# Kernel optimization log

Hardware: AMD Instinct MI355X
Metric: run time of the kernel (lower is better)

Reference implementation:

```python
import jax, jax.numpy as jnp
import numpy as np

MAX_DIM = 1024
VOCAB = 257
DEPTH = 6
Q_DIM = MAX_DIM // 4  # 256
EXP_DIMS = [1, 2, 4, 8, 16, 32, 64, 128]  # expander sizes: current_q doubles up to Q_DIM
BATCH, SEQ = 8, 4096


def qlinear(q, W):
    """Quaternion Hamilton-product linear.
    q: [..., in, 4] (last dim = r,i,j,k components), W: [4, out, in] (stacked r,i,j,k weights).
    Returns [..., out, 4].
    """
    # P[..., o, w, a] = F.linear(component_a, W_w)  -> all 16 small GEMMs in one einsum
    P = jnp.einsum('...ia,woi->...owa', q, W)
    Pr, Pi, Pj, Pk = P[..., 0, :], P[..., 1, :], P[..., 2, :], P[..., 3, :]  # each [..., out, 4]
    out_r = Pr[..., 0] - Pi[..., 1] - Pj[..., 2] - Pk[..., 3]
    out_i = Pi[..., 0] + Pr[..., 1] + Pk[..., 2] - Pj[..., 3]
    out_j = Pj[..., 0] - Pk[..., 1] + Pr[..., 2] + Pi[..., 3]
    out_k = Pk[..., 0] + Pj[..., 1] - Pi[..., 2] + Pr[..., 3]
    return jnp.stack([out_r, out_i, out_j, out_k], axis=-1)


def qnormalize(q):
    norm = jnp.linalg.norm(q, axis=-1, keepdims=True)
    return q / (norm + 1e-8)


def setup_inputs() -> dict:
    key = jax.random.key(0)
    ks = jax.random.split(key, 4 + len(EXP_DIMS))
    inp = {}
    inp['x'] = jax.random.randint(ks[0], (BATCH, SEQ), 0, VOCAB)
    inp['emb'] = jax.random.normal(ks[1], (VOCAB, 4), dtype=jnp.float32)
    for idx, cq in enumerate(EXP_DIMS):
        scale = cq ** (-0.5)
        inp[f'w_exp{idx}'] = jax.random.uniform(ks[2 + idx], (4, cq, cq), jnp.float32, -scale, scale)
    scale = Q_DIM ** (-0.5)
    inp['w_layers'] = jax.random.uniform(ks[-2], (DEPTH, 4, Q_DIM, Q_DIM), jnp.float32, -scale, scale)
    inp['w_head'] = jax.random.normal(ks[-1], (VOCAB, MAX_DIM), dtype=jnp.float32) * MAX_DIM ** (-0.5)
    return inp


def reference(x, emb, w_exp0, w_exp1, w_exp2, w_exp3, w_exp4, w_exp5, w_exp6, w_exp7,
              w_layers, w_head):
    q = emb[x][:, :, None, :]  # [B, S, 1, 4]
    for w in (w_exp0, w_exp1, w_exp2, w_exp3, w_exp4, w_exp5, w_exp6, w_exp7):
        delta = jnp.tanh(qlinear(q, w))
        q = jnp.concatenate([q + delta, q - delta], axis=2)  # doubles quaternion dim
    for d in range(DEPTH):
        q = qnormalize(qlinear(q, w_layers[d]))
    stability_loss = jnp.mean(jnp.abs(q[..., 0]))
    h_flat = q.reshape(x.shape[0], x.shape[1], -1)  # [B, S, MAX_DIM]
    logits = jnp.einsum('bsd,vd->bsv', h_flat, w_head)
    return (logits, stability_loss)
```

## Files before the change

kernel.cpp:

```cpp
#include <hip/hip_runtime.h>


typedef _Float16 f16x8 __attribute__((ext_vector_type(8)));
typedef float    f32x4 __attribute__((ext_vector_type(4)));

#define GL2LDS16(gp, lp) __builtin_amdgcn_global_load_lds(                     \
    (const __attribute__((address_space(1))) void*)(gp),                       \
    (__attribute__((address_space(3))) void*)(lp), 16, 0, 0)

__device__ __forceinline__ unsigned short f2h(float f) {
  union { _Float16 h; unsigned short u; } c;
  c.h = (_Float16)f;
  return c.u;
}
__device__ __forceinline__ float h2f(unsigned short u) {
  union { unsigned short u; _Float16 h; } c;
  c.u = u;
  return (float)c.h;
}

__global__ __launch_bounds__(256) void expand_ham(
    const float* __restrict__ w, unsigned short* __restrict__ out,
    int cq, int kbits, int total) {
  int id = blockIdx.x * 256 + threadIdx.x;
  if (id >= total) return;
  const int K = 1 << kbits;
  const int n = id >> kbits;
  const int k = id & (K - 1);
  float val = 0.f;
  if (n < 4 * cq) {
    const int o = n >> 2, a = n & 3, i = k >> 2, b = k & 3;
    const int   comp[4][4] = {{0,1,2,3},{1,0,3,2},{2,3,0,1},{3,2,1,0}};
    const float sgn [4][4] = {{1.f,-1.f,-1.f,-1.f},{1.f,1.f,1.f,-1.f},
                              {1.f,-1.f,1.f,1.f},{1.f,1.f,-1.f,1.f}};
    val = sgn[a][b] * w[comp[a][b] * cq * cq + o * cq + i];
  }
  out[id] = f2h(val);
}

__global__ __launch_bounds__(256) void conv_head(
    const float* __restrict__ wh, unsigned short* __restrict__ out) {
  int id = blockIdx.x * 256 + threadIdx.x;
  int v = id >> 10, k = id & 1023;
  out[id] = f2h(v < 257 ? wh[v * 1024 + k] : 0.f);
}

template <int CQ>
__device__ __forceinline__ void exp_step(float (&q)[16][4],
                                         const float* __restrict__ w) {
  float d[CQ][4];
#pragma unroll
  for (int o = 0; o < CQ; o++) {
    float pr = 0.f, pi = 0.f, pj = 0.f, pk = 0.f;
#pragma unroll
    for (int i = 0; i < CQ; i++) {
      const float wr = w[0 * CQ * CQ + o * CQ + i];
      const float wi = w[1 * CQ * CQ + o * CQ + i];
      const float wj = w[2 * CQ * CQ + o * CQ + i];
      const float wk = w[3 * CQ * CQ + o * CQ + i];
      const float qr = q[i][0], qi = q[i][1], qj = q[i][2], qk = q[i][3];
      pr += wr * qr - wi * qi - wj * qj - wk * qk;
      pi += wi * qr + wr * qi + wk * qj - wj * qk;
      pj += wj * qr - wk * qi + wr * qj + wi * qk;
      pk += wk * qr + wj * qi - wi * qj + wr * qk;
    }
    d[o][0] = tanhf(pr); d[o][1] = tanhf(pi);
    d[o][2] = tanhf(pj); d[o][3] = tanhf(pk);
  }
#pragma unroll
  for (int o = 0; o < CQ; o++)
#pragma unroll
    for (int a = 0; a < 4; a++) {
      const float dd = d[o][a], qq = q[o][a];
      q[o][a]      = qq + dd;
      q[CQ + o][a] = qq - dd;
    }
}

__global__ __launch_bounds__(256) void embed_expand(
    const int* __restrict__ x, const float* __restrict__ emb,
    const float* __restrict__ w0, const float* __restrict__ w1,
    const float* __restrict__ w2, const float* __restrict__ w3,
    unsigned short* __restrict__ out) {
  const int t = blockIdx.x * 256 + threadIdx.x;
  float q[16][4];
  const int v = x[t];
  const float4 e = *(const float4*)(emb + v * 4);
  q[0][0] = e.x; q[0][1] = e.y; q[0][2] = e.z; q[0][3] = e.w;
  exp_step<1>(q, w0);
  exp_step<2>(q, w1);
  exp_step<4>(q, w2);
  exp_step<8>(q, w3);
  ushort4* o4 = (ushort4*)(out + (size_t)t * 64);
#pragma unroll
  for (int c = 0; c < 16; c++) {
    ushort4 u;
    u.x = f2h(q[c][0]); u.y = f2h(q[c][1]);
    u.z = f2h(q[c][2]); u.w = f2h(q[c][3]);
    o4[c] = u;
  }
}

template <int EPI>
__global__ __launch_bounds__(256) void gemm_epi(
    const unsigned short* __restrict__ W,
    const unsigned short* __restrict__ Act,
    unsigned short* __restrict__ OutB, float* __restrict__ OutF,
    int K, int Nreal, int ldout) {
  __shared__ unsigned short WtL[128 * 32];
  __shared__ unsigned short WtH[128 * 32];
  __shared__ unsigned short AtL[128 * 32];
  __shared__ unsigned short AtH[128 * 32];

  const int tid  = threadIdx.x;
  const int wave = tid >> 6;
  const int lane = tid & 63;
  const int l15  = lane & 15;
  const int quad = lane >> 4;

  const int Gx = gridDim.x;
  const int L  = blockIdx.y * Gx + blockIdx.x;
  const int j  = L & 7;
  const int s  = L >> 3;
  const int nblock = (s % Gx) * 128;
  const int mblock = (32 * j + s / Gx) * 128;
  const int wn = (wave & 1) * 64;
  const int wm = (wave >> 1) * 64;

  f32x4 acc[4][4];
  const f32x4 zero = {0.f, 0.f, 0.f, 0.f};
#pragma unroll
  for (int a = 0; a < 4; a++)
#pragma unroll
    for (int b = 0; b < 4; b++) acc[a][b] = zero;

  const int row0 = tid >> 2;
  const int sub  = tid & 3;
  const unsigned short* gW0 = W   + (size_t)(nblock + row0)      * K + sub * 8;
  const unsigned short* gW1 = W   + (size_t)(nblock + row0 + 64) * K + sub * 8;
  const unsigned short* gA0 = Act + (size_t)(mblock + row0)      * K + sub * 8;
  const unsigned short* gA1 = Act + (size_t)(mblock + row0 + 64) * K + sub * 8;
  unsigned short* lWL0 = &WtL[wave * 512];
  unsigned short* lWL1 = &WtL[2048 + wave * 512];
  unsigned short* lWH0 = &WtH[wave * 512];
  unsigned short* lWH1 = &WtH[2048 + wave * 512];
  unsigned short* lAL0 = &AtL[wave * 512];
  unsigned short* lAL1 = &AtL[2048 + wave * 512];
  unsigned short* lAH0 = &AtH[wave * 512];
  unsigned short* lAH1 = &AtH[2048 + wave * 512];

  for (int kb = 0; kb < K; kb += 64) {
    GL2LDS16(gW0 + kb,      lWL0);
    GL2LDS16(gW1 + kb,      lWL1);
    GL2LDS16(gW0 + kb + 32, lWH0);
    GL2LDS16(gW1 + kb + 32, lWH1);
    GL2LDS16(gA0 + kb,      lAL0);
    GL2LDS16(gA1 + kb,      lAL1);
    GL2LDS16(gA0 + kb + 32, lAH0);
    GL2LDS16(gA1 + kb + 32, lAH1);
    __syncthreads();

    {
      f16x8 afr[4], bfr[4];
#pragma unroll
      for (int tn = 0; tn < 4; tn++)
        afr[tn] = *(const f16x8*)&WtL[(wn + tn * 16 + l15) * 32 + quad * 8];
#pragma unroll
      for (int tm = 0; tm < 4; tm++)
        bfr[tm] = *(const f16x8*)&AtL[(wm + tm * 16 + l15) * 32 + quad * 8];
#pragma unroll
      for (int tn = 0; tn < 4; tn++)
#pragma unroll
        for (int tm = 0; tm < 4; tm++)
          acc[tn][tm] = __builtin_amdgcn_mfma_f32_16x16x32_f16(
              afr[tn], bfr[tm], acc[tn][tm], 0, 0, 0);
    }
    {
      f16x8 afr[4], bfr[4];
#pragma unroll
      for (int tn = 0; tn < 4; tn++)
        afr[tn] = *(const f16x8*)&WtH[(wn + tn * 16 + l15) * 32 + quad * 8];
#pragma unroll
      for (int tm = 0; tm < 4; tm++)
        bfr[tm] = *(const f16x8*)&AtH[(wm + tm * 16 + l15) * 32 + quad * 8];
#pragma unroll
      for (int tn = 0; tn < 4; tn++)
#pragma unroll
        for (int tm = 0; tm < 4; tm++)
          acc[tn][tm] = __builtin_amdgcn_mfma_f32_16x16x32_f16(
              afr[tn], bfr[tm], acc[tn][tm], 0, 0, 0);
    }
    __syncthreads();
  }

#pragma unroll
  for (int tn = 0; tn < 4; tn++) {
    const int n = nblock + wn + tn * 16 + quad * 4;
    if (n < Nreal) {
#pragma unroll
      for (int tm = 0; tm < 4; tm++) {
        const int token = mblock + wm + tm * 16 + l15;
        const f32x4 v = acc[tn][tm];
        const unsigned short* ip = Act + (size_t)token * K + n;
        const float i0 = h2f(ip[0]), i1 = h2f(ip[1]);
        const float i2 = h2f(ip[2]), i3 = h2f(ip[3]);
        const float d0 = tanhf(v[0]), d1 = tanhf(v[1]);
        const float d2 = tanhf(v[2]), d3 = tanhf(v[3]);
        ushort4 up, um;
        up.x = f2h(i0 + d0); up.y = f2h(i1 + d1);
        up.z = f2h(i2 + d2); up.w = f2h(i3 + d3);
        um.x = f2h(i0 - d0); um.y = f2h(i1 - d1);
        um.z = f2h(i2 - d2); um.w = f2h(i3 - d3);
        *(ushort4*)&OutB[(size_t)token * ldout + n] = up;
        *(ushort4*)&OutB[(size_t)token * ldout + Nreal + n] = um;
      }
    }
  }
}

template <int EPI>
__global__ __launch_bounds__(512, 4) void gemm8p(
    const unsigned short* __restrict__ W,
    const unsigned short* __restrict__ Act,
    unsigned short* __restrict__ OutB, float* __restrict__ OutF,
    int K, int NW, int ldout) {
  __shared__ unsigned short S[3 * 12288];
  __shared__ float lsum[8];

  const int tid  = threadIdx.x;
  const int wave = tid >> 6;
  const int lane = tid & 63;
  const int l15  = lane & 15;
  const int quad = lane >> 4;
  const int wr   = wave >> 2;
  const int wc   = wave & 3;

  const int Gx = gridDim.x;
  const int L  = blockIdx.y * Gx + blockIdx.x;
  const int j  = L & 7;
  const int s  = L >> 3;
  const int mblock = (j * (gridDim.y >> 3) + s / Gx) * 256;
  const int nblock = (s % Gx) * 128;
  const int NT = K >> 5;

  f32x4 acc[4][4];
  const f32x4 zero = {0.f, 0.f, 0.f, 0.f};
#pragma unroll
  for (int a = 0; a < 4; a++)
#pragma unroll
    for (int b = 0; b < 4; b++) acc[a][b] = zero;

  const int rw = tid >> 2;
  const int sl = (tid & 3) ^ ((tid >> 3) & 3);
  const int wrow = nblock + rw;
  const int cwr  = wrow < NW ? wrow : NW - 1;
  const unsigned short* sW  = W   + (size_t)cwr * K + sl * 8;
  const unsigned short* sB0 = Act + (size_t)(mblock + rw)       * K + sl * 8;
  const unsigned short* sB1 = Act + (size_t)(mblock + 128 + rw) * K + sl * 8;

  const int swz = (quad * 8) ^ ((l15 & 6) << 2);

#pragma unroll
  for (int t = 0; t < 2; ++t) {
    unsigned short* d = S + t * 12288 + tid * 8;
    GL2LDS16(sW  + t * 32, d);
    GL2LDS16(sB0 + t * 32, d + 4096);
    GL2LDS16(sB1 + t * 32, d + 8192);
  }
  asm volatile("s_waitcnt vmcnt(3)" ::: "memory");
  __builtin_amdgcn_s_barrier();
  __builtin_amdgcn_sched_barrier(0);

  int bC = 0;
  int bS = 2;
  for (int kt = 0; kt < NT; ++kt) {
    const unsigned short* SA = S + bC * 12288;
    const unsigned short* SB = SA + 4096;

    f16x8 af[4], bf[4];
#pragma unroll
    for (int t4 = 0; t4 < 4; t4++)
      af[t4] = *(const f16x8*)(SA + (wr * 64 + t4 * 16 + l15) * 32 + swz);
#pragma unroll
    for (int t4 = 0; t4 < 4; t4++)
      bf[t4] = *(const f16x8*)(SB + (wc * 64 + t4 * 16 + l15) * 32 + swz);

    if (kt + 2 < NT) {
      const int kb = (kt + 2) * 32;
      unsigned short* d = S + bS * 12288 + tid * 8;
      GL2LDS16(sW  + kb, d);
      GL2LDS16(sB0 + kb, d + 4096);
      GL2LDS16(sB1 + kb, d + 8192);
    }

    __builtin_amdgcn_s_barrier();
    asm volatile("s_waitcnt lgkmcnt(0)" ::: "memory");
    __builtin_amdgcn_sched_barrier(0);
    __builtin_amdgcn_s_setprio(1);
#pragma unroll
    for (int tn = 0; tn < 4; tn++)
#pragma unroll
      for (int tm = 0; tm < 4; tm++)
        acc[tn][tm] = __builtin_amdgcn_mfma_f32_16x16x32_f16(
            af[tn], bf[tm], acc[tn][tm], 0, 0, 0);
    __builtin_amdgcn_s_setprio(0);

    if (kt < NT - 1) {
      if (kt + 2 < NT) asm volatile("s_waitcnt vmcnt(3)" ::: "memory");
      else             asm volatile("s_waitcnt vmcnt(0)" ::: "memory");
      __builtin_amdgcn_s_barrier();
      __builtin_amdgcn_sched_barrier(0);
    }
    bC = bC == 2 ? 0 : bC + 1;
    bS = bS == 2 ? 0 : bS + 1;
  }

  if constexpr (EPI == 0) {
#pragma unroll
    for (int tn = 0; tn < 4; tn++) {
      const int n = nblock + wr * 64 + tn * 16 + quad * 4;
#pragma unroll
      for (int tm = 0; tm < 4; tm++) {
        const int token = mblock + wc * 64 + tm * 16 + l15;
        const f32x4 v = acc[tn][tm];
        const unsigned short* ip = Act + (size_t)token * K + n;
        const float i0 = h2f(ip[0]), i1 = h2f(ip[1]);
        const float i2 = h2f(ip[2]), i3 = h2f(ip[3]);
        const float d0 = tanhf(v[0]), d1 = tanhf(v[1]);
        const float d2 = tanhf(v[2]), d3 = tanhf(v[3]);
        ushort4 up, um;
        up.x = f2h(i0 + d0); up.y = f2h(i1 + d1);
        up.z = f2h(i2 + d2); up.w = f2h(i3 + d3);
        um.x = f2h(i0 - d0); um.y = f2h(i1 - d1);
        um.z = f2h(i2 - d2); um.w = f2h(i3 - d3);
        *(ushort4*)&OutB[(size_t)token * ldout + n] = up;
        *(ushort4*)&OutB[(size_t)token * ldout + NW + n] = um;
      }
    }
  } else if constexpr (EPI == 1 || EPI == 2) {
    float loss = 0.f;
#pragma unroll
    for (int tn = 0; tn < 4; tn++) {
      const int n = nblock + wr * 64 + tn * 16 + quad * 4;
#pragma unroll
      for (int tm = 0; tm < 4; tm++) {
        const int token = mblock + wc * 64 + tm * 16 + l15;
        const f32x4 v = acc[tn][tm];
        const float nrm =
            sqrtf(v[0] * v[0] + v[1] * v[1] + v[2] * v[2] + v[3] * v[3]);
        const float inv = 1.f / (nrm + 1e-8f);
        ushort4 u;
        u.x = f2h(v[0] * inv); u.y = f2h(v[1] * inv);
        u.z = f2h(v[2] * inv); u.w = f2h(v[3] * inv);
        *(ushort4*)&OutB[(size_t)token * 1024 + n] = u;
        if constexpr (EPI == 2) loss += fabsf(v[0] * inv);
      }
    }
    if constexpr (EPI == 2) {
#pragma unroll
      for (int off = 32; off > 0; off >>= 1) loss += __shfl_down(loss, off);
      if (lane == 0) lsum[wave] = loss;
      __syncthreads();
      if (tid == 0) {
        float t = 0.f;
#pragma unroll
        for (int w8 = 0; w8 < 8; w8++) t += lsum[w8];
        atomicAdd(OutF, t * (1.f / 8388608.f));
      }
    }
  } else {
#pragma unroll
    for (int tn = 0; tn < 4; tn++) {
      const int n = nblock + wr * 64 + tn * 16 + quad * 4;
      if (n < 257) {
#pragma unroll
        for (int tm = 0; tm < 4; tm++) {
          const int token = mblock + wc * 64 + tm * 16 + l15;
          const f32x4 v = acc[tn][tm];
#pragma unroll
          for (int r = 0; r < 4; r++)
            if (n + r < 257) OutF[(size_t)token * 257 + n + r] = v[r];
        }
      }
    }
  }
}

extern "C" void kernel_launch(void* const* d_in, const int* in_sizes, int n_in,
                              void* d_out, int out_size, void* d_ws,
                              size_t ws_size, hipStream_t stream) {
  const int*   x    = (const int*)d_in[0];
  const float* emb  = (const float*)d_in[1];
  const float* we0  = (const float*)d_in[2];
  const float* we1  = (const float*)d_in[3];
  const float* we2  = (const float*)d_in[4];
  const float* we3  = (const float*)d_in[5];
  const float* we4  = (const float*)d_in[6];
  const float* we5  = (const float*)d_in[7];
  const float* we6  = (const float*)d_in[8];
  const float* we7  = (const float*)d_in[9];
  const float* wlay = (const float*)d_in[10];
  const float* wh   = (const float*)d_in[11];
  float* out = (float*)d_out;

  char* p = (char*)d_ws;
  auto alloc = [&](size_t bytes) {
    void* r = (void*)p;
    p += (bytes + 255) & ~(size_t)255;
    return r;
  };
  unsigned short* act0 = (unsigned short*)alloc(32768ull * 1024 * 2);
  unsigned short* act1 = (unsigned short*)alloc(32768ull * 1024 * 2);
  unsigned short* E4 = (unsigned short*)alloc(128 * 64 * 2);
  unsigned short* E5 = (unsigned short*)alloc(128 * 128 * 2);
  unsigned short* E6 = (unsigned short*)alloc(256 * 256 * 2);
  unsigned short* E7 = (unsigned short*)alloc(512 * 512 * 2);
  unsigned short* EL = (unsigned short*)alloc(6ull * 1024 * 1024 * 2);
  unsigned short* WH = (unsigned short*)alloc(384 * 1024 * 2);

  hipMemsetAsync(out + 8421376, 0, 4, stream);

  expand_ham<<<dim3(8192 / 256), 256, 0, stream>>>(we4, E4, 16, 6, 128 * 64);
  expand_ham<<<dim3(16384 / 256), 256, 0, stream>>>(we5, E5, 32, 7, 128 * 128);
  expand_ham<<<dim3(65536 / 256), 256, 0, stream>>>(we6, E6, 64, 8, 256 * 256);
  expand_ham<<<dim3(262144 / 256), 256, 0, stream>>>(we7, E7, 128, 9,
                                                     512 * 512);
  for (int d = 0; d < 6; d++)
    expand_ham<<<dim3(1048576 / 256), 256, 0, stream>>>(
        wlay + (size_t)d * 262144, EL + (size_t)d * 1048576, 256, 10, 1048576);
  conv_head<<<dim3(384 * 1024 / 256), 256, 0, stream>>>(wh, WH);

  embed_expand<<<dim3(128), 256, 0, stream>>>(x, emb, we0, we1, we2, we3, act0);

  gemm_epi<0><<<dim3(1, 256), 256, 0, stream>>>(E4, act0, act1, nullptr, 64,
                                                64, 128);
  gemm_epi<0><<<dim3(1, 256), 256, 0, stream>>>(E5, act1, act0, nullptr, 128,
                                                128, 256);
  gemm8p<0><<<dim3(2, 128), 512, 0, stream>>>(E6, act0, act1, nullptr, 256,
                                              256, 512);
  gemm8p<0><<<dim3(4, 128), 512, 0, stream>>>(E7, act1, act0, nullptr, 512,
                                              512, 1024);

  unsigned short* a = act0;
  unsigned short* b = act1;
  for (int d = 0; d < 5; d++) {
    gemm8p<1><<<dim3(8, 128), 512, 0, stream>>>(EL + (size_t)d * 1048576, a, b,
                                                nullptr, 1024, 1024, 1024);
    unsigned short* t = a; a = b; b = t;
  }
  gemm8p<2><<<dim3(8, 128), 512, 0, stream>>>(EL + 5ull * 1048576, a, b,
                                              out + 8421376, 1024, 1024, 1024);
  { unsigned short* t = a; a = b; b = t; }

  gemm8p<3><<<dim3(3, 128), 512, 0, stream>>>(WH, a, nullptr, out, 1024, 384,
                                              0);
}
```

Before: 832.7 us.

## Shrink gemm8p tile to 128x128 with 4 waves and double-buffered LDS

Restructures the main GEMM kernel from 512-thread blocks on a 128x256 tile with triple-buffered LDS to 256-thread blocks on a 128x128 tile with double buffering. The grid doubles in the M dimension and each thread loads two W rows and two activation rows. The barrier now comes before the next prefetch so the buffer being refilled is safe. The aim is more resident blocks per CU and less LDS per block, at the cost of less reuse per tile and one fewer stage of prefetch slack. It also merges the six layer-weight expansion launches into a single kernel.

```diff
diff --git a/kernel.cpp b/kernel.cpp
--- a/kernel.cpp
+++ b/kernel.cpp
@@ -35,6 +35,21 @@
                               {1.f,-1.f,1.f,1.f},{1.f,1.f,-1.f,1.f}};
     val = sgn[a][b] * w[comp[a][b] * cq * cq + o * cq + i];
   }
+  out[id] = f2h(val);
+}
+
+__global__ __launch_bounds__(256) void expand_ham6(
+    const float* __restrict__ w, unsigned short* __restrict__ out) {
+  const int id = blockIdx.x * 256 + threadIdx.x;
+  const int d = id >> 20;
+  const int r = id & 1048575;
+  const int n = r >> 10, k = r & 1023;
+  const int o = n >> 2, a = n & 3, i = k >> 2, b = k & 3;
+  const int   comp[4][4] = {{0,1,2,3},{1,0,3,2},{2,3,0,1},{3,2,1,0}};
+  const float sgn [4][4] = {{1.f,-1.f,-1.f,-1.f},{1.f,1.f,1.f,-1.f},
+                            {1.f,-1.f,1.f,1.f},{1.f,1.f,-1.f,1.f}};
+  const float val =
+      sgn[a][b] * w[d * 262144 + comp[a][b] * 65536 + o * 256 + i];
   out[id] = f2h(val);
 }
 
@@ -219,27 +234,27 @@
 }
 
 template <int EPI>
-__global__ __launch_bounds__(512, 4) void gemm8p(
+__global__ __launch_bounds__(256, 4) void gemm8p(
     const unsigned short* __restrict__ W,
     const unsigned short* __restrict__ Act,
     unsigned short* __restrict__ OutB, float* __restrict__ OutF,
     int K, int NW, int ldout) {
-  __shared__ unsigned short S[3 * 12288];
-  __shared__ float lsum[8];
+  __shared__ unsigned short S[2 * 8192];
+  __shared__ float lsum[4];
 
   const int tid  = threadIdx.x;
   const int wave = tid >> 6;
   const int lane = tid & 63;
   const int l15  = lane & 15;
   const int quad = lane >> 4;
-  const int wr   = wave >> 2;
-  const int wc   = wave & 3;
+  const int wr   = wave >> 1;
+  const int wc   = wave & 1;
 
   const int Gx = gridDim.x;
   const int L  = blockIdx.y * Gx + blockIdx.x;
   const int j  = L & 7;
   const int s  = L >> 3;
-  const int mblock = (j * (gridDim.y >> 3) + s / Gx) * 256;
+  const int mblock = (j * (gridDim.y >> 3) + s / Gx) * 128;
   const int nblock = (s % Gx) * 128;
   const int NT = K >> 5;
 
@@ -252,29 +267,40 @@
 
   const int rw = tid >> 2;
   const int sl = (tid & 3) ^ ((tid >> 3) & 3);
-  const int wrow = nblock + rw;
-  const int cwr  = wrow < NW ? wrow : NW - 1;
-  const unsigned short* sW  = W   + (size_t)cwr * K + sl * 8;
-  const unsigned short* sB0 = Act + (size_t)(mblock + rw)       * K + sl * 8;
-  const unsigned short* sB1 = Act + (size_t)(mblock + 128 + rw) * K + sl * 8;
+  const int wrow0 = nblock + rw;
+  const int wrow1 = nblock + 64 + rw;
+  const int cw0 = wrow0 < NW ? wrow0 : NW - 1;
+  const int cw1 = wrow1 < NW ? wrow1 : NW - 1;
+  const unsigned short* sW0 = W   + (size_t)cw0 * K + sl * 8;
+  const unsigned short* sW1 = W   + (size_t)cw1 * K + sl * 8;
+  const unsigned short* sB0 = Act + (size_t)(mblock + rw)      * K + sl * 8;
+  const unsigned short* sB1 = Act + (size_t)(mblock + 64 + rw) * K + sl * 8;
 
   const int swz = (quad * 8) ^ ((l15 & 6) << 2);
 
-#pragma unroll
-  for (int t = 0; t < 2; ++t) {
-    unsigned short* d = S + t * 12288 + tid * 8;
-    GL2LDS16(sW  + t * 32, d);
-    GL2LDS16(sB0 + t * 32, d + 4096);
-    GL2LDS16(sB1 + t * 32, d + 8192);
-  }
-  asm volatile("s_waitcnt vmcnt(3)" ::: "memory");
+  {
+    unsigned short* d0 = S + tid * 8;
+    GL2LDS16(sW0, d0);
+    GL2LDS16(sW1, d0 + 2048);
+    GL2LDS16(sB0, d0 + 4096);
+    GL2LDS16(sB1, d0 + 6144);
+    if (NT > 1) {
+      unsigned short* d1 = S + 8192 + tid * 8;
+      GL2LDS16(sW0 + 32, d1);
+      GL2LDS16(sW1 + 32, d1 + 2048);
+      GL2LDS16(sB0 + 32, d1 + 4096);
+      GL2LDS16(sB1 + 32, d1 + 6144);
+      asm volatile("s_waitcnt vmcnt(4)" ::: "memory");
+    } else {
+      asm volatile("s_waitcnt vmcnt(0)" ::: "memory");
+    }
+  }
   __builtin_amdgcn_s_barrier();
   __builtin_amdgcn_sched_barrier(0);
 
-  int bC = 0;
-  int bS = 2;
+#pragma unroll 2
   for (int kt = 0; kt < NT; ++kt) {
-    const unsigned short* SA = S + bC * 12288;
+    const unsigned short* SA = S + (kt & 1) * 8192;
     const unsigned short* SB = SA + 4096;
 
     f16x8 af[4], bf[4];
@@ -285,17 +311,18 @@
     for (int t4 = 0; t4 < 4; t4++)
       bf[t4] = *(const f16x8*)(SB + (wc * 64 + t4 * 16 + l15) * 32 + swz);
 
+    asm volatile("s_waitcnt lgkmcnt(0)" ::: "memory");
+    __builtin_amdgcn_s_barrier();
+    __builtin_amdgcn_sched_barrier(0);
     if (kt + 2 < NT) {
       const int kb = (kt + 2) * 32;
-      unsigned short* d = S + bS * 12288 + tid * 8;
-      GL2LDS16(sW  + kb, d);
+      unsigned short* d = S + (kt & 1) * 8192 + tid * 8;
+      GL2LDS16(sW0 + kb, d);
+      GL2LDS16(sW1 + kb, d + 2048);
       GL2LDS16(sB0 + kb, d + 4096);
-      GL2LDS16(sB1 + kb, d + 8192);
-    }
-
-    __builtin_amdgcn_s_barrier();
-    asm volatile("s_waitcnt lgkmcnt(0)" ::: "memory");
-    __builtin_amdgcn_sched_barrier(0);
+      GL2LDS16(sB1 + kb, d + 6144);
+    }
+
     __builtin_amdgcn_s_setprio(1);
 #pragma unroll
     for (int tn = 0; tn < 4; tn++)
@@ -306,13 +333,11 @@
     __builtin_amdgcn_s_setprio(0);
 
     if (kt < NT - 1) {
-      if (kt + 2 < NT) asm volatile("s_waitcnt vmcnt(3)" ::: "memory");
+      if (kt + 2 < NT) asm volatile("s_waitcnt vmcnt(4)" ::: "memory");
       else             asm volatile("s_waitcnt vmcnt(0)" ::: "memory");
       __builtin_amdgcn_s_barrier();
       __builtin_amdgcn_sched_barrier(0);
     }
-    bC = bC == 2 ? 0 : bC + 1;
-    bS = bS == 2 ? 0 : bS + 1;
   }
 
   if constexpr (EPI == 0) {
@@ -362,9 +387,7 @@
       if (lane == 0) lsum[wave] = loss;
       __syncthreads();
       if (tid == 0) {
-        float t = 0.f;
-#pragma unroll
-        for (int w8 = 0; w8 < 8; w8++) t += lsum[w8];
+        float t = lsum[0] + lsum[1] + lsum[2] + lsum[3];
         atomicAdd(OutF, t * (1.f / 8388608.f));
       }
     }
@@ -425,9 +448,7 @@
   expand_ham<<<dim3(65536 / 256), 256, 0, stream>>>(we6, E6, 64, 8, 256 * 256);
   expand_ham<<<dim3(262144 / 256), 256, 0, stream>>>(we7, E7, 128, 9,
                                                      512 * 512);
-  for (int d = 0; d < 6; d++)
-    expand_ham<<<dim3(1048576 / 256), 256, 0, stream>>>(
-        wlay + (size_t)d * 262144, EL + (size_t)d * 1048576, 256, 10, 1048576);
+  expand_ham6<<<dim3(6 * 1048576 / 256), 256, 0, stream>>>(wlay, EL);
   conv_head<<<dim3(384 * 1024 / 256), 256, 0, stream>>>(wh, WH);
 
   embed_expand<<<dim3(128), 256, 0, stream>>>(x, emb, we0, we1, we2, we3, act0);
@@ -436,22 +457,22 @@
                                                 64, 128);
   gemm_epi<0><<<dim3(1, 256), 256, 0, stream>>>(E5, act1, act0, nullptr, 128,
                                                 128, 256);
-  gemm8p<0><<<dim3(2, 128), 512, 0, stream>>>(E6, act0, act1, nullptr, 256,
+  gemm8p<0><<<dim3(2, 256), 256, 0, stream>>>(E6, act0, act1, nullptr, 256,
                                               256, 512);
-  gemm8p<0><<<dim3(4, 128), 512, 0, stream>>>(E7, act1, act0, nullptr, 512,
+  gemm8p<0><<<dim3(4, 256), 256, 0, stream>>>(E7, act1, act0, nullptr, 512,
                                               512, 1024);
 
   unsigned short* a = act0;
   unsigned short* b = act1;
   for (int d = 0; d < 5; d++) {
-    gemm8p<1><<<dim3(8, 128), 512, 0, stream>>>(EL + (size_t)d * 1048576, a, b,
+    gemm8p<1><<<dim3(8, 256), 256, 0, stream>>>(EL + (size_t)d * 1048576, a, b,
                                                 nullptr, 1024, 1024, 1024);
     unsigned short* t = a; a = b; b = t;
   }
-  gemm8p<2><<<dim3(8, 128), 512, 0, stream>>>(EL + 5ull * 1048576, a, b,
+  gemm8p<2><<<dim3(8, 256), 256, 0, stream>>>(EL + 5ull * 1048576, a, b,
                                               out + 8421376, 1024, 1024, 1024);
   { unsigned short* t = a; a = b; b = t; }
 
-  gemm8p<3><<<dim3(3, 128), 512, 0, stream>>>(WH, a, nullptr, out, 1024, 384,
+  gemm8p<3><<<dim3(3, 256), 256, 0, stream>>>(WH, a, nullptr, out, 1024, 384,
                                               0);
 }
```

Measured after the change: 973.9 us. 17.0% more time.

## Add dedicated triple-buffered head GEMM and merge layer weight expansion launches

Applied to the files above, without the earlier changes.

Replaces the generic gemm8p head path with a dedicated gemm_head kernel. The new kernel uses a three-stage LDS ring fed by direct global-to-LDS loads with prefetch distance two, swizzled LDS reads, and launch bounds of 512 threads with 4 blocks. It also merges the six per-layer expand_ham launches into one expand_ham6 launch and trims the unused epilogue template from the small GEMM. The aim is to overlap the head's loads with MFMA work and to cut launch overhead, at the cost of more LDS use and duplicated GEMM code.

```diff
diff --git a/kernel.cpp b/kernel.cpp
--- a/kernel.cpp
+++ b/kernel.cpp
@@ -38,6 +38,21 @@
   out[id] = f2h(val);
 }
 
+__global__ __launch_bounds__(256) void expand_ham6(
+    const float* __restrict__ w, unsigned short* __restrict__ out) {
+  const int id = blockIdx.x * 256 + threadIdx.x;
+  const int d = id >> 20;
+  const int r = id & 1048575;
+  const int n = r >> 10, k = r & 1023;
+  const int o = n >> 2, a = n & 3, i = k >> 2, b = k & 3;
+  const int   comp[4][4] = {{0,1,2,3},{1,0,3,2},{2,3,0,1},{3,2,1,0}};
+  const float sgn [4][4] = {{1.f,-1.f,-1.f,-1.f},{1.f,1.f,1.f,-1.f},
+                            {1.f,-1.f,1.f,1.f},{1.f,1.f,-1.f,1.f}};
+  const float val =
+      sgn[a][b] * w[d * 262144 + comp[a][b] * 65536 + o * 256 + i];
+  out[id] = f2h(val);
+}
+
 __global__ __launch_bounds__(256) void conv_head(
     const float* __restrict__ wh, unsigned short* __restrict__ out) {
   int id = blockIdx.x * 256 + threadIdx.x;
@@ -101,11 +116,10 @@
   }
 }
 
-template <int EPI>
-__global__ __launch_bounds__(256) void gemm_epi(
+__global__ __launch_bounds__(256) void gemm_epi0(
     const unsigned short* __restrict__ W,
     const unsigned short* __restrict__ Act,
-    unsigned short* __restrict__ OutB, float* __restrict__ OutF,
+    unsigned short* __restrict__ OutB,
     int K, int Nreal, int ldout) {
   __shared__ unsigned short WtL[128 * 32];
   __shared__ unsigned short WtH[128 * 32];
@@ -337,7 +351,7 @@
         *(ushort4*)&OutB[(size_t)token * ldout + NW + n] = um;
       }
     }
-  } else if constexpr (EPI == 1 || EPI == 2) {
+  } else {
     float loss = 0.f;
 #pragma unroll
     for (int tn = 0; tn < 4; tn++) {
@@ -368,19 +382,112 @@
         atomicAdd(OutF, t * (1.f / 8388608.f));
       }
     }
-  } else {
-#pragma unroll
-    for (int tn = 0; tn < 4; tn++) {
-      const int n = nblock + wr * 64 + tn * 16 + quad * 4;
-      if (n < 257) {
-#pragma unroll
-        for (int tm = 0; tm < 4; tm++) {
-          const int token = mblock + wc * 64 + tm * 16 + l15;
-          const f32x4 v = acc[tn][tm];
-#pragma unroll
-          for (int r = 0; r < 4; r++)
-            if (n + r < 257) OutF[(size_t)token * 257 + n + r] = v[r];
-        }
+  }
+}
+
+__global__ __launch_bounds__(512, 4) void gemm_head(
+    const unsigned short* __restrict__ W,
+    const unsigned short* __restrict__ Act,
+    float* __restrict__ OutF, int K) {
+  __shared__ unsigned short S[3 * 12288];
+
+  const int tid  = threadIdx.x;
+  const int wave = tid >> 6;
+  const int lane = tid & 63;
+  const int l15  = lane & 15;
+  const int quad = lane >> 4;
+  const int wr   = wave >> 2;
+  const int wc   = wave & 3;
+
+  const int Gx = gridDim.x;
+  const int L  = blockIdx.y * Gx + blockIdx.x;
+  const int j  = L & 7;
+  const int s  = L >> 3;
+  const int mblock = (j * (gridDim.y >> 3) + s / Gx) * 256;
+  const int nblock = (s % Gx) * 128;
+  const int NT = K >> 5;
+
+  f32x4 acc[4][4];
+  const f32x4 zero = {0.f, 0.f, 0.f, 0.f};
+#pragma unroll
+  for (int a = 0; a < 4; a++)
+#pragma unroll
+    for (int b = 0; b < 4; b++) acc[a][b] = zero;
+
+  const int rw = tid >> 2;
+  const int sl = (tid & 3) ^ ((tid >> 3) & 3);
+  const unsigned short* sW  = W   + (size_t)(nblock + rw) * K + sl * 8;
+  const unsigned short* sB0 = Act + (size_t)(mblock + rw)       * K + sl * 8;
+  const unsigned short* sB1 = Act + (size_t)(mblock + 128 + rw) * K + sl * 8;
+
+  const int swz = (quad * 8) ^ ((l15 & 6) << 2);
+
+#pragma unroll
+  for (int t = 0; t < 2; ++t) {
+    unsigned short* d = S + t * 12288 + tid * 8;
+    GL2LDS16(sW  + t * 32, d);
+    GL2LDS16(sB0 + t * 32, d + 4096);
+    GL2LDS16(sB1 + t * 32, d + 8192);
+  }
+  asm volatile("s_waitcnt vmcnt(3)" ::: "memory");
+  __builtin_amdgcn_s_barrier();
+  __builtin_amdgcn_sched_barrier(0);
+
+  int bC = 0;
+  int bS = 2;
+  for (int kt = 0; kt < NT; ++kt) {
+    const unsigned short* SA = S + bC * 12288;
+    const unsigned short* SB = SA + 4096;
+
+    f16x8 af[4], bf[4];
+#pragma unroll
+    for (int t4 = 0; t4 < 4; t4++)
+      af[t4] = *(const f16x8*)(SA + (wr * 64 + t4 * 16 + l15) * 32 + swz);
+#pragma unroll
+    for (int t4 = 0; t4 < 4; t4++)
+      bf[t4] = *(const f16x8*)(SB + (wc * 64 + t4 * 16 + l15) * 32 + swz);
+
+    if (kt + 2 < NT) {
+      const int kb = (kt + 2) * 32;
+      unsigned short* d = S + bS * 12288 + tid * 8;
+      GL2LDS16(sW  + kb, d);
+      GL2LDS16(sB0 + kb, d + 4096);
+      GL2LDS16(sB1 + kb, d + 8192);
+    }
+
+    __builtin_amdgcn_s_barrier();
+    asm volatile("s_waitcnt lgkmcnt(0)" ::: "memory");
+    __builtin_amdgcn_sched_barrier(0);
+    __builtin_amdgcn_s_setprio(1);
+#pragma unroll
+    for (int tn = 0; tn < 4; tn++)
+#pragma unroll
+      for (int tm = 0; tm < 4; tm++)
+        acc[tn][tm] = __builtin_amdgcn_mfma_f32_16x16x32_f16(
+            af[tn], bf[tm], acc[tn][tm], 0, 0, 0);
+    __builtin_amdgcn_s_setprio(0);
+
+    if (kt < NT - 1) {
+      if (kt + 2 < NT) asm volatile("s_waitcnt vmcnt(3)" ::: "memory");
+      else             asm volatile("s_waitcnt vmcnt(0)" ::: "memory");
+      __builtin_amdgcn_s_barrier();
+      __builtin_amdgcn_sched_barrier(0);
+    }
+    bC = bC == 2 ? 0 : bC + 1;
+    bS = bS == 2 ? 0 : bS + 1;
+  }
+
+#pragma unroll
+  for (int tn = 0; tn < 4; tn++) {
+    const int n = nblock + wr * 64 + tn * 16 + quad * 4;
+    if (n < 257) {
+#pragma unroll
+      for (int tm = 0; tm < 4; tm++) {
+        const int token = mblock + wc * 64 + tm * 16 + l15;
+        const f32x4 v = acc[tn][tm];
+#pragma unroll
+        for (int r = 0; r < 4; r++)
+          if (n + r < 257) OutF[(size_t)token * 257 + n + r] = v[r];
       }
     }
   }
@@ -425,17 +532,13 @@
   expand_ham<<<dim3(65536 / 256), 256, 0, stream>>>(we6, E6, 64, 8, 256 * 256);
   expand_ham<<<dim3(262144 / 256), 256, 0, stream>>>(we7, E7, 128, 9,
                                                      512 * 512);
-  for (int d = 0; d < 6; d++)
-    expand_ham<<<dim3(1048576 / 256), 256, 0, stream>>>(
-        wlay + (size_t)d * 262144, EL + (size_t)d * 1048576, 256, 10, 1048576);
+  expand_ham6<<<dim3(6 * 1048576 / 256), 256, 0, stream>>>(wlay, EL);
   conv_head<<<dim3(384 * 1024 / 256), 256, 0, stream>>>(wh, WH);
 
   embed_expand<<<dim3(128), 256, 0, stream>>>(x, emb, we0, we1, we2, we3, act0);
 
-  gemm_epi<0><<<dim3(1, 256), 256, 0, stream>>>(E4, act0, act1, nullptr, 64,
-                                                64, 128);
-  gemm_epi<0><<<dim3(1, 256), 256, 0, stream>>>(E5, act1, act0, nullptr, 128,
-                                                128, 256);
+  gemm_epi0<<<dim3(1, 256), 256, 0, stream>>>(E4, act0, act1, 64, 64, 128);
+  gemm_epi0<<<dim3(1, 256), 256, 0, stream>>>(E5, act1, act0, 128, 128, 256);
   gemm8p<0><<<dim3(2, 128), 512, 0, stream>>>(E6, act0, act1, nullptr, 256,
                                               256, 512);
   gemm8p<0><<<dim3(4, 128), 512, 0, stream>>>(E7, act1, act0, nullptr, 512,
@@ -452,6 +555,5 @@
                                               out + 8421376, 1024, 1024, 1024);
   { unsigned short* t = a; a = b; b = t; }
 
-  gemm8p<3><<<dim3(3, 128), 512, 0, stream>>>(WH, a, nullptr, out, 1024, 384,
-                                              0);
-}
+  gemm_head<<<dim3(3, 128), 512, 0, stream>>>(WH, a, out, 1024);
+}
```

New measurement: 932.8 us. 1.12x slower.
